# Performance work log

Measured on AMD Instinct MI355X. Metric: run time of the kernel, lower is better.

## Reference

```python
import jax, jax.numpy as jnp
import numpy as np


def setup_inputs() -> dict:
    key = jax.random.key(0)
    kx, ky = jax.random.split(key)
    n, m, d = 2048, 2048, 16  # d == n_wires
    x = jax.random.normal(kx, (n, d), dtype=jnp.float32)
    y = jax.random.normal(ky, (m, d), dtype=jnp.float32)
    return {"x": x, "y": y}


def reference(x, y):
    # RY gates on distinct wires commute; RY(-y_k) RY(x_k) = RY(x_k - y_k).
    # State = tensor product over wires of RY(x_k - y_k)|0>, so the |0...0>
    # amplitude is prod_k cos((x_k - y_k)/2). Original code stores abs(amplitude).
    half_diff = 0.5 * (x[:, None, :] - y[None, :, :])  # [n, m, d]
    kernel = jnp.abs(jnp.prod(jnp.cos(half_diff), axis=-1))  # [n, m]
    return kernel
```

## Files before the change

kernel.cpp:

```cpp
#include <hip/hip_runtime.h>
#include <hip/hip_bf16.h>


constexpr int D  = 16;
constexpr int RPB = 16;
constexpr int CPW = 128;

typedef float vf2 __attribute__((ext_vector_type(2)));

__global__ __launch_bounds__(256)
void precs(const float* __restrict__ x, const float* __restrict__ y,
           float2* __restrict__ csx, float2* __restrict__ csy_t,
           int nx, int m) {
    const int gid = blockIdx.x * 256 + threadIdx.x;
    if (gid < nx) {
        float s, c;
        __sincosf(0.5f * x[gid], &s, &c);
        csx[gid] = make_float2(c, s);
    } else {
        const int j = gid - nx;
        const int k = j / m, col = j - k * m;
        float s, c;
        __sincosf(0.5f * y[(size_t)col * D + k], &s, &c);
        csy_t[j] = make_float2(c, s);
    }
}

__global__ __launch_bounds__(64)
void qkern(const float2* __restrict__ csx, const float2* __restrict__ csy_t,
           float* __restrict__ out, int m) {
    const int lane = threadIdx.x;
    const int col0 = blockIdx.x * CPW + lane * 2;
    const int rbase = blockIdx.y * RPB;

    float4 colf[D];
#pragma unroll
    for (int k = 0; k < D; ++k)
        colf[k] = *(const float4*)(csy_t + (size_t)k * m + col0);

    const float2* rp = csx + (size_t)rbase * D;

#pragma unroll 4
    for (int i = 0; i < RPB; ++i) {
        float p0 = 1.0f, p1 = 1.0f;
#pragma unroll
        for (int k = 0; k < D; ++k) {
            const float cxk = rp[i * D + k].x;
            const float sxk = rp[i * D + k].y;
            const float t0 = cxk * colf[k].x + sxk * colf[k].y;
            const float t1 = cxk * colf[k].z + sxk * colf[k].w;
            p0 *= t0;
            p1 *= t1;
        }
        vf2 v;
        v.x = fabsf(p0);
        v.y = fabsf(p1);
        __builtin_nontemporal_store(
            v, (vf2*)(out + (size_t)(rbase + i) * m + col0));
    }
}

extern "C" void kernel_launch(void* const* d_in, const int* in_sizes, int n_in,
                              void* d_out, int out_size, void* d_ws, size_t ws_size,
                              hipStream_t stream) {
    const float* x = (const float*)d_in[0];
    const float* y = (const float*)d_in[1];
    float* out = (float*)d_out;
    const int n = in_sizes[0] / D;
    const int m = in_sizes[1] / D;

    float2* csx   = (float2*)d_ws;
    float2* csy_t = (float2*)d_ws + (size_t)n * D;

    const int nx = n * D, ny = m * D;
    precs<<<(nx + ny + 255) / 256, 256, 0, stream>>>(x, y, csx, csy_t, nx, m);

    dim3 grid(m / CPW, n / RPB);
    qkern<<<grid, 64, 0, stream>>>(csx, csy_t, out, m);
}
```

Baseline: 73.93 us.

## Recast per-pair cosine products as bf16 MFMA dot products over wire pairs

The wires are grouped into pairs, and the product of two cos(a-b) factors is expanded into a 4-term dot product. Two such pairs then combine into a 16-term bf16 dot product, so each group of four wires becomes one 16x16x32 MFMA slice. The precompute kernel builds bf16 feature vectors for rows and columns, and the main kernel multiplies four MFMA results elementwise. This moves the scalar FMA inner loop onto matrix cores. The cost is bf16 rounding of the features and half-zeroed MFMA operands, which could reduce accuracy.

```diff
diff --git a/kernel.cpp b/kernel.cpp
--- a/kernel.cpp
+++ b/kernel.cpp
@@ -2,61 +2,98 @@
 #include <hip/hip_bf16.h>
 
 
-constexpr int D  = 16;
-constexpr int RPB = 16;
-constexpr int CPW = 128;
+constexpr int D = 16;
 
-typedef float vf2 __attribute__((ext_vector_type(2)));
+typedef short  bf16x8 __attribute__((ext_vector_type(8)));
+typedef float  f32x4  __attribute__((ext_vector_type(4)));
+
+static __device__ inline unsigned int pk2(float a, float b) {
+    __hip_bfloat16 ha = __float2bfloat16(a);
+    __hip_bfloat16 hb = __float2bfloat16(b);
+    unsigned short ua, ub;
+    __builtin_memcpy(&ua, &ha, 2);
+    __builtin_memcpy(&ub, &hb, 2);
+    return (unsigned int)ua | ((unsigned int)ub << 16);
+}
 
 __global__ __launch_bounds__(256)
 void precs(const float* __restrict__ x, const float* __restrict__ y,
-           float2* __restrict__ csx, float2* __restrict__ csy_t,
-           int nx, int m) {
-    const int gid = blockIdx.x * 256 + threadIdx.x;
-    if (gid < nx) {
-        float s, c;
-        __sincosf(0.5f * x[gid], &s, &c);
-        csx[gid] = make_float2(c, s);
-    } else {
-        const int j = gid - nx;
-        const int k = j / m, col = j - k * m;
-        float s, c;
-        __sincosf(0.5f * y[(size_t)col * D + k], &s, &c);
-        csy_t[j] = make_float2(c, s);
+           unsigned short* __restrict__ Arow, unsigned short* __restrict__ Bcol,
+           int n, int ntot) {
+    const int u = blockIdx.x * 256 + threadIdx.x;
+    if (u >= ntot) return;
+    const bool isrow = (u < n);
+    const float* src = isrow ? (x + (size_t)u * D) : (y + (size_t)(u - n) * D);
+    unsigned short* dst =
+        isrow ? (Arow + (size_t)u * 64) : (Bcol + (size_t)(u - n) * 64);
+    const float scale = isrow ? 0.5f : 1.0f;
+
+    float f[8][4];
+#pragma unroll
+    for (int p = 0; p < 8; ++p) {
+        const float a0 = src[2 * p], a1 = src[2 * p + 1];
+        float sm, cm, sp, cp;
+        __sincosf(0.5f * (a0 - a1), &sm, &cm);
+        __sincosf(0.5f * (a0 + a1), &sp, &cp);
+        f[p][0] = scale * cm; f[p][1] = scale * sm;
+        f[p][2] = scale * cp; f[p][3] = scale * sp;
+    }
+#pragma unroll
+    for (int q = 0; q < 4; ++q) {
+        uint4 lo, hi;
+        lo.x = pk2(f[2*q][0]*f[2*q+1][0], f[2*q][0]*f[2*q+1][1]);
+        lo.y = pk2(f[2*q][0]*f[2*q+1][2], f[2*q][0]*f[2*q+1][3]);
+        lo.z = pk2(f[2*q][1]*f[2*q+1][0], f[2*q][1]*f[2*q+1][1]);
+        lo.w = pk2(f[2*q][1]*f[2*q+1][2], f[2*q][1]*f[2*q+1][3]);
+        hi.x = pk2(f[2*q][2]*f[2*q+1][0], f[2*q][2]*f[2*q+1][1]);
+        hi.y = pk2(f[2*q][2]*f[2*q+1][2], f[2*q][2]*f[2*q+1][3]);
+        hi.z = pk2(f[2*q][3]*f[2*q+1][0], f[2*q][3]*f[2*q+1][1]);
+        hi.w = pk2(f[2*q][3]*f[2*q+1][2], f[2*q][3]*f[2*q+1][3]);
+        *(uint4*)(dst + q * 16)     = lo;
+        *(uint4*)(dst + q * 16 + 8) = hi;
     }
 }
 
-__global__ __launch_bounds__(64)
-void qkern(const float2* __restrict__ csx, const float2* __restrict__ csy_t,
+__global__ __launch_bounds__(256)
+void qkern(const unsigned short* __restrict__ Arow,
+           const unsigned short* __restrict__ Bcol,
            float* __restrict__ out, int m) {
-    const int lane = threadIdx.x;
-    const int col0 = blockIdx.x * CPW + lane * 2;
-    const int rbase = blockIdx.y * RPB;
+    const int tid  = threadIdx.x;
+    const int wave = tid >> 6;
+    const int lane = tid & 63;
+    const int m16  = lane & 15;
+    const int half = lane >> 4;
+    const int row0 = blockIdx.x * 64 + wave * 16;
+    const int col0 = blockIdx.y * 64;
 
-    float4 colf[D];
+    const bf16x8 zf = {0, 0, 0, 0, 0, 0, 0, 0};
+    const f32x4  zc = {0.f, 0.f, 0.f, 0.f};
+
+    bf16x8 af[4];
 #pragma unroll
-    for (int k = 0; k < D; ++k)
-        colf[k] = *(const float4*)(csy_t + (size_t)k * m + col0);
+    for (int q = 0; q < 4; ++q)
+        af[q] = (half < 2)
+            ? *(const bf16x8*)(Arow + (size_t)(row0 + m16) * 64 + q * 16 + half * 8)
+            : zf;
 
-    const float2* rp = csx + (size_t)rbase * D;
-
-#pragma unroll 4
-    for (int i = 0; i < RPB; ++i) {
-        float p0 = 1.0f, p1 = 1.0f;
 #pragma unroll
-        for (int k = 0; k < D; ++k) {
-            const float cxk = rp[i * D + k].x;
-            const float sxk = rp[i * D + k].y;
-            const float t0 = cxk * colf[k].x + sxk * colf[k].y;
-            const float t1 = cxk * colf[k].z + sxk * colf[k].w;
-            p0 *= t0;
-            p1 *= t1;
+    for (int cg = 0; cg < 4; ++cg) {
+        const int colb = col0 + cg * 16;
+        f32x4 acc[4];
+#pragma unroll
+        for (int q = 0; q < 4; ++q) {
+            const bf16x8 bfq = (half < 2)
+                ? *(const bf16x8*)(Bcol + (size_t)(colb + m16) * 64 + q * 16 + half * 8)
+                : zf;
+            acc[q] = __builtin_amdgcn_mfma_f32_16x16x32_bf16(af[q], bfq, zc, 0, 0, 0);
         }
-        vf2 v;
-        v.x = fabsf(p0);
-        v.y = fabsf(p1);
-        __builtin_nontemporal_store(
-            v, (vf2*)(out + (size_t)(rbase + i) * m + col0));
+#pragma unroll
+        for (int r = 0; r < 4; ++r) {
+            const float v =
+                fabsf(acc[0][r] * acc[1][r] * acc[2][r] * acc[3][r]);
+            const int row = row0 + half * 4 + r;
+            __builtin_nontemporal_store(v, out + (size_t)row * m + colb + m16);
+        }
     }
 }
 
@@ -69,12 +106,12 @@
     const int n = in_sizes[0] / D;
     const int m = in_sizes[1] / D;
 
-    float2* csx   = (float2*)d_ws;
-    float2* csy_t = (float2*)d_ws + (size_t)n * D;
+    unsigned short* Arow = (unsigned short*)d_ws;
+    unsigned short* Bcol = Arow + (size_t)n * 64;
 
-    const int nx = n * D, ny = m * D;
-    precs<<<(nx + ny + 255) / 256, 256, 0, stream>>>(x, y, csx, csy_t, nx, m);
+    const int ntot = n + m;
+    precs<<<(ntot + 255) / 256, 256, 0, stream>>>(x, y, Arow, Bcol, n, ntot);
 
-    dim3 grid(m / CPW, n / RPB);
-    qkern<<<grid, 64, 0, stream>>>(csx, csy_t, out, m);
+    dim3 grid(n / 64, m / 64);
+    qkern<<<grid, 256, 0, stream>>>(Arow, Bcol, out, m);
 }
```

Result: faster. 68.78 us (-7.0%).
